# Performance work log

Measured on AMD Instinct MI355X. Metric: run time of the kernel, lower is better.

## Reference

```python
import jax, jax.numpy as jnp
import numpy as np

T = 3          # hparams['T'] message-passing iterations
E = 100000     # num edges (rows of link_state)
M = 200000     # num message pairs
D = 128        # hidden dim of link_state / GRU units
H = 256        # Message MLP hidden width
G = 64         # num graphs


def setup_inputs() -> dict:
    key = jax.random.key(0)
    ks = jax.random.split(key, 16)
    s = 0.05
    inp = {
        'link_state': jax.random.normal(ks[0], (E, D), jnp.float32),
        'states_first': jax.random.randint(ks[1], (M,), 0, E),
        'states_second': jax.random.randint(ks[2], (M,), 0, E),
        'states_graph_ids': jnp.sort(jax.random.randint(ks[3], (E,), 0, G)),
        'sates_num_edges': E,
        # Message MLP: Dense(H, relu) -> Dense(D, relu)
        'mW1': jax.random.normal(ks[4], (2 * D, H), jnp.float32) * s,
        'mb1': jnp.zeros((H,), jnp.float32),
        'mW2': jax.random.normal(ks[5], (H, D), jnp.float32) * s,
        'mb2': jnp.zeros((D,), jnp.float32),
        # GRUCell (keras, reset_after=True): kernel [D,3D], recurrent [D,3D], bias [2,3D]
        'gru_kernel': jax.random.normal(ks[6], (D, 3 * D), jnp.float32) * s,
        'gru_recurrent': jax.random.normal(ks[7], (D, 3 * D), jnp.float32) * s,
        'gru_bias': jnp.zeros((2, 3 * D), jnp.float32),
        # Readout MLP: Dense(H, relu) -> Dense(H, relu) -> Dense(1)
        'rW1': jax.random.normal(ks[8], (D, H), jnp.float32) * s,
        'rb1': jnp.zeros((H,), jnp.float32),
        'rW2': jax.random.normal(ks[9], (H, H), jnp.float32) * s,
        'rb2': jnp.zeros((H,), jnp.float32),
        'rW3': jax.random.normal(ks[10], (H, 1), jnp.float32) * s,
        'rb3': jnp.zeros((1,), jnp.float32),
    }
    return inp


def _gru_step(x, h, kernel, recurrent, bias):
    # keras GRUCell with reset_after=True; gate order: z, r, h
    mx = x @ kernel + bias[0]          # [N, 3D]
    mh = h @ recurrent + bias[1]       # [N, 3D]
    xz, xr, xh = jnp.split(mx, 3, axis=-1)
    hz, hr, hh = jnp.split(mh, 3, axis=-1)
    z = jax.nn.sigmoid(xz + hz)
    r = jax.nn.sigmoid(xr + hr)
    hcand = jnp.tanh(xh + r * hh)
    return z * h + (1.0 - z) * hcand


def reference(link_state, states_first, states_second, states_graph_ids,
              sates_num_edges, mW1, mb1, mW2, mb2,
              gru_kernel, gru_recurrent, gru_bias,
              rW1, rb1, rW2, rb2, rW3, rb3):
    for _ in range(T):
        main_e = link_state[states_first]        # [M, D] gather
        neigh_e = link_state[states_second]      # [M, D] gather
        concat = jnp.concatenate([main_e, neigh_e], axis=1)  # [M, 2D]
        msg = jax.nn.relu(concat @ mW1 + mb1)
        msg = jax.nn.relu(msg @ mW2 + mb2)       # [M, D]
        edges_inputs = jax.ops.segment_sum(msg, states_second,
                                           num_segments=sates_num_edges)  # [E, D]
        link_state = _gru_step(edges_inputs, link_state,
                               gru_kernel, gru_recurrent, gru_bias)
    graph_state = jax.ops.segment_sum(link_state, states_graph_ids,
                                      num_segments=G)  # [G, D]
    r = jax.nn.relu(graph_state @ rW1 + rb1)
    r = jax.nn.relu(r @ rW2 + rb2)
    return r @ rW3 + rb3  # [G, 1]
```

## Files before the change

### kernel.cpp

```cpp
#include <hip/hip_runtime.h>

#define NUM_E 100000
#define NUM_M 200000
#define DIM   128
#define HID   256
#define NG    64
#define TITER 3
#define NB_SCAN 98
#define GS_ER 128
#define TM    64

typedef __attribute__((ext_vector_type(8))) short bf16x8;
typedef __attribute__((ext_vector_type(4))) float f32x4;

__device__ __forceinline__ unsigned short f2bf(float f) {
  unsigned u = __float_as_uint(f);
  u += 0x7FFF + ((u >> 16) & 1);
  return (unsigned short)(u >> 16);
}
__device__ __forceinline__ float bf2f(unsigned short h) {
  return __uint_as_float(((unsigned)h) << 16);
}
__device__ __forceinline__ float sigmoidf_(float v) {
  return 1.f / (1.f + __expf(-v));
}
__device__ __forceinline__ float tanhf_(float u) {
  u = fminf(fmaxf(u, -15.f), 15.f);
  float ex = __expf(-2.f * u);
  return (1.f - ex) / (1.f + ex);
}
__device__ __forceinline__ float relu_(float v) { return fmaxf(v, 0.f); }

__device__ __forceinline__ void acc8(float* xs, bf16x8 v) {
  #pragma unroll
  for (int j = 0; j < 8; ++j) xs[j] += bf2f((unsigned short)v[j]);
}

__device__ __forceinline__ int swzm(int row, int col) {
  return row * 256 + (col ^ ((row & 7) << 3));
}
__device__ __forceinline__ int swzg(int row, int col) {
  return row * 128 + (col ^ ((row & 7) << 3));
}

#define MFMA(a, b, c) __builtin_amdgcn_mfma_f32_16x16x32_bf16((a), (b), (c), 0, 0, 0)

__global__ void hist_kernel(const int* __restrict__ second, int* __restrict__ counts,
                            float4* __restrict__ gs4) {
  int m = blockIdx.x * blockDim.x + threadIdx.x;
  if (m < NG * DIM / 4) gs4[m] = make_float4(0.f, 0.f, 0.f, 0.f);
  if (m < NUM_M) atomicAdd(&counts[second[m]], 1);
}

__global__ __launch_bounds__(256) void scan1_kernel(const int* __restrict__ counts,
                                                    int* __restrict__ partials) {
  __shared__ int sh[256];
  int b = blockIdx.x, t = threadIdx.x;
  int i0 = b * 1024 + t * 4;
  int c0 = (i0 + 0 < NUM_E) ? counts[i0 + 0] : 0;
  int c1 = (i0 + 1 < NUM_E) ? counts[i0 + 1] : 0;
  int c2 = (i0 + 2 < NUM_E) ? counts[i0 + 2] : 0;
  int c3 = (i0 + 3 < NUM_E) ? counts[i0 + 3] : 0;
  int tsum = c0 + c1 + c2 + c3;
  sh[t] = tsum;
  __syncthreads();
  for (int off = 1; off < 256; off <<= 1) {
    int v = (t >= off) ? sh[t - off] : 0;
    __syncthreads();
    sh[t] += v;
    __syncthreads();
  }
  if (t == 255) partials[b] = sh[255];
}

__global__ void scan2_kernel(const int* __restrict__ partials, int* __restrict__ base,
                             int* __restrict__ rowptr) {
  if (threadIdx.x == 0) {
    int run = 0;
    for (int b = 0; b < NB_SCAN; ++b) { base[b] = run; run += partials[b]; }
    rowptr[NUM_E] = NUM_M;
  }
}

__global__ __launch_bounds__(256) void scan3_kernel(const int* __restrict__ counts,
                                                    const int* __restrict__ base,
                                                    int* __restrict__ rowptr) {
  __shared__ int sh[256];
  int b = blockIdx.x, t = threadIdx.x;
  int i0 = b * 1024 + t * 4;
  int c0 = (i0 + 0 < NUM_E) ? counts[i0 + 0] : 0;
  int c1 = (i0 + 1 < NUM_E) ? counts[i0 + 1] : 0;
  int c2 = (i0 + 2 < NUM_E) ? counts[i0 + 2] : 0;
  int c3 = (i0 + 3 < NUM_E) ? counts[i0 + 3] : 0;
  int tsum = c0 + c1 + c2 + c3;
  sh[t] = tsum;
  __syncthreads();
  for (int off = 1; off < 256; off <<= 1) {
    int v = (t >= off) ? sh[t - off] : 0;
    __syncthreads();
    sh[t] += v;
    __syncthreads();
  }
  int p = base[b] + (sh[t] - tsum);
  if (i0 + 0 < NUM_E) rowptr[i0 + 0] = p;
  if (i0 + 1 < NUM_E) rowptr[i0 + 1] = p + c0;
  if (i0 + 2 < NUM_E) rowptr[i0 + 2] = p + c0 + c1;
  if (i0 + 3 < NUM_E) rowptr[i0 + 3] = p + c0 + c1 + c2;
}

__global__ void scatter_kernel(const int* __restrict__ second,
                               const int* __restrict__ rowptr,
                               int* __restrict__ cursor, int* __restrict__ order) {
  int m = blockIdx.x * blockDim.x + threadIdx.x;
  if (m < NUM_M) {
    int e = second[m];
    int pos = atomicAdd(&cursor[e], 1);
    int idx = rowptr[e] + pos;
    if (idx < rowptr[e + 1]) order[idx] = m;
  }
}

__device__ __forceinline__ void pack_range(
    const float* __restrict__ srcA, const float* __restrict__ srcB, int KrowsA,
    int N, int src_ld, int col_off, unsigned short* __restrict__ dst, int idx) {
  int l = idx & 63;
  int t = idx >> 6;
  int NF = N / 16;
  int nf = t % NF;
  int ks = t / NF;
  int n = nf * 16 + (l & 15) + col_off;
  int k0 = ks * 32 + (l >> 4) * 8;
  unsigned short o[8];
  #pragma unroll
  for (int j = 0; j < 8; ++j) {
    int k = k0 + j;
    const float* src = (k < KrowsA) ? (srcA + (size_t)k * src_ld)
                                    : (srcB + (size_t)(k - KrowsA) * src_ld);
    o[j] = f2bf(src[n]);
  }
  ushort4* d = (ushort4*)(dst + (size_t)idx * 8);
  d[0] = make_ushort4(o[0], o[1], o[2], o[3]);
  d[1] = make_ushort4(o[4], o[5], o[6], o[7]);
}

__global__ __launch_bounds__(256) void prep_kernel(
    const float4* __restrict__ ls4, ushort4* __restrict__ lsb4, int n4,
    const float* __restrict__ mW1, const float* __restrict__ mW2,
    const float* __restrict__ gk,  const float* __restrict__ gr,
    unsigned short* __restrict__ W1p,  unsigned short* __restrict__ W2p,
    unsigned short* __restrict__ Wzrp, unsigned short* __restrict__ Wkhp,
    unsigned short* __restrict__ Wrhp) {
  int i = blockIdx.x * 256 + threadIdx.x;
  if (i < n4) {
    float4 v = ls4[i];
    ushort4 o;
    o.x = f2bf(v.x); o.y = f2bf(v.y); o.z = f2bf(v.z); o.w = f2bf(v.w);
    lsb4[i] = o;
  }
  if      (i < 8192)  pack_range(mW1, mW1, 256, 256, 256, 0,   W1p,  i);
  else if (i < 12288) pack_range(mW2, mW2, 256, 128, 128, 0,   W2p,  i - 8192);
  else if (i < 20480) pack_range(gk,  gr,  128, 256, 384, 0,   Wzrp, i - 12288);
  else if (i < 22528) pack_range(gk,  gk,  128, 128, 384, 256, Wkhp, i - 20480);
  else if (i < 24576) pack_range(gr,  gr,  128, 128, 384, 256, Wrhp, i - 22528);
}

__global__ __launch_bounds__(512, 2) void msg_kernel(
    const unsigned short* __restrict__ lsb,
    const int* __restrict__ first, const int* __restrict__ second,
    const int* __restrict__ order,
    const unsigned short* __restrict__ W1p,
    const float* __restrict__ b1,
    const unsigned short* __restrict__ W2p,
    const float* __restrict__ b2,
    unsigned short* __restrict__ msgout)
{
  __shared__ unsigned short actL[2][TM * 256];
  __shared__ unsigned short h1s[2][TM * 256];

  const int tid  = threadIdx.x;
  const int wave = tid >> 6;
  const int lane = tid & 63;
  const int c    = lane & 15;
  const int quad = lane >> 4;

  const int sr  = tid >> 5;
  const int shf = (tid >> 4) & 1;
  const int si  = tid & 15;

  const bf16x8* W1f = (const bf16x8*)W1p;
  const bf16x8* W2f = (const bf16x8*)W2p;
  bf16x8 w1r[16];
  #pragma unroll
  for (int ks = 0; ks < 8; ++ks)
    #pragma unroll
    for (int i = 0; i < 2; ++i)
      w1r[ks * 2 + i] = W1f[(ks * 16 + wave * 2 + i) * 64 + lane];
  bf16x8 w2r[8];
  #pragma unroll
  for (int ks = 0; ks < 8; ++ks)
    w2r[ks] = W2f[(ks * 8 + wave) * 64 + lane];

  float4 b1v[2];
  #pragma unroll
  for (int i = 0; i < 2; ++i)
    b1v[i] = *(const float4*)(b1 + (wave * 2 + i) * 16 + quad * 4);
  float4 b2v = *(const float4*)(b2 + wave * 16 + quad * 4);

  const int nTiles = NUM_M / TM;
  const int stride = gridDim.x;
  int tile = blockIdx.x;
  if (tile >= nTiles) return;
  int parity = 0;

  {
    #pragma unroll
    for (int k = 0; k < 4; ++k) {
      int m = order[tile * TM + sr + k * 16];
      int e = shf ? second[m] : first[m];
      bf16x8 v = *(const bf16x8*)(lsb + (size_t)e * DIM + si * 8);
      *(bf16x8*)&actL[0][swzm(sr + k * 16, shf * 128 + si * 8)] = v;
    }
  }
  int en[4] = {0, 0, 0, 0};
  {
    int t1 = tile + stride;
    if (t1 < nTiles) {
      #pragma unroll
      for (int k = 0; k < 4; ++k) {
        int m = order[t1 * TM + sr + k * 16];
        en[k] = shf ? second[m] : first[m];
      }
    }
  }
  __syncthreads();

  while (true) {
    const int m0 = tile * TM;
    const int next  = tile + stride;
    const int next2 = next + stride;
    const bool have_next  = (next < nTiles);
    const bool have_next2 = (next2 < nTiles);

    bf16x8 sv[4];
    if (have_next) {
      #pragma unroll
      for (int k = 0; k < 4; ++k)
        sv[k] = *(const bf16x8*)(lsb + (size_t)en[k] * DIM + si * 8);
    }
    int o[4] = {0, 0, 0, 0};
    if (have_next2) {
      #pragma unroll
      for (int k = 0; k < 4; ++k)
        o[k] = order[next2 * TM + sr + k * 16];
    }

    const unsigned short* ab = &actL[parity][0];
    f32x4 acc[4][2];
    #pragma unroll
    for (int s = 0; s < 4; ++s) { acc[s][0] = (f32x4)(0.f); acc[s][1] = (f32x4)(0.f); }
    #pragma unroll
    for (int ks = 0; ks < 8; ++ks) {
      #pragma unroll
      for (int s = 0; s < 4; ++s) {
        bf16x8 b = *(const bf16x8*)&ab[swzm(s * 16 + c, ks * 32 + quad * 8)];
        acc[s][0] = MFMA(w1r[ks * 2 + 0], b, acc[s][0]);
        acc[s][1] = MFMA(w1r[ks * 2 + 1], b, acc[s][1]);
      }
    }

    if (have_next2) {
      #pragma unroll
      for (int k = 0; k < 4; ++k)
        en[k] = shf ? second[o[k]] : first[o[k]];
    }

    if (have_next) {
      unsigned short* aw = &actL[parity ^ 1][0];
      #pragma unroll
      for (int k = 0; k < 4; ++k)
        *(bf16x8*)&aw[swzm(sr + k * 16, shf * 128 + si * 8)] = sv[k];
    }

    unsigned short* hb = &h1s[parity][0];
    #pragma unroll
    for (int i = 0; i < 2; ++i) {
      int n0 = (wave * 2 + i) * 16 + quad * 4;
      #pragma unroll
      for (int s = 0; s < 4; ++s) {
        ushort4 pk;
        pk.x = f2bf(relu_(acc[s][i][0] + b1v[i].x));
        pk.y = f2bf(relu_(acc[s][i][1] + b1v[i].y));
        pk.z = f2bf(relu_(acc[s][i][2] + b1v[i].z));
        pk.w = f2bf(relu_(acc[s][i][3] + b1v[i].w));
        *(ushort4*)&hb[swzm(s * 16 + c, n0)] = pk;
      }
    }
    __syncthreads();

    f32x4 a2[4];
    #pragma unroll
    for (int s = 0; s < 4; ++s) a2[s] = (f32x4)(0.f);
    #pragma unroll
    for (int ks2 = 0; ks2 < 8; ++ks2) {
      #pragma unroll
      for (int s = 0; s < 4; ++s) {
        bf16x8 b = *(const bf16x8*)&hb[swzm(s * 16 + c, ks2 * 32 + quad * 8)];
        a2[s] = MFMA(w2r[ks2], b, a2[s]);
      }
    }

    {
      int n0 = wave * 16 + quad * 4;
      #pragma unroll
      for (int s = 0; s < 4; ++s) {
        ushort4 pk;
        pk.x = f2bf(relu_(a2[s][0] + b2v.x));
        pk.y = f2bf(relu_(a2[s][1] + b2v.y));
        pk.z = f2bf(relu_(a2[s][2] + b2v.z));
        pk.w = f2bf(relu_(a2[s][3] + b2v.w));
        *(ushort4*)(msgout + (size_t)(m0 + s * 16 + c) * DIM + n0) = pk;
      }
    }

    if (!have_next) break;
    tile = next;
    parity ^= 1;
  }
}

__device__ __forceinline__ ushort4 gru_gate(
    f32x4 az, f32x4 ar, f32x4 axh, f32x4 ahh, ushort4 hraw,
    float4 bz0, float4 br0, float4 bh0, float4 bz1, float4 br1, float4 bh1) {
  float ho[4] = { bf2f(hraw.x), bf2f(hraw.y), bf2f(hraw.z), bf2f(hraw.w) };
  const float* paz  = (const float*)&az;  const float* par  = (const float*)&ar;
  const float* paxh = (const float*)&axh; const float* pahh = (const float*)&ahh;
  const float* pz0 = (const float*)&bz0; const float* pr0 = (const float*)&br0;
  const float* ph0 = (const float*)&bh0; const float* pz1 = (const float*)&bz1;
  const float* pr1 = (const float*)&br1; const float* ph1 = (const float*)&bh1;
  unsigned short o[4];
  #pragma unroll
  for (int j = 0; j < 4; ++j) {
    float z  = sigmoidf_(paz[j] + pz0[j] + pz1[j]);
    float r  = sigmoidf_(par[j] + pr0[j] + pr1[j]);
    float hc = tanhf_(paxh[j] + ph0[j] + r * (pahh[j] + ph1[j]));
    o[j] = f2bf(z * ho[j] + (1.f - z) * hc);
  }
  return make_ushort4(o[0], o[1], o[2], o[3]);
}

__global__ __launch_bounds__(512, 2) void gru_kernel(
    const unsigned short* __restrict__ msgb,
    const int* __restrict__ rowptr,
    unsigned short* __restrict__ lsb,
    const unsigned short* __restrict__ Wzrp,
    const unsigned short* __restrict__ Wkhp,
    const unsigned short* __restrict__ Wrhp,
    const float* __restrict__ gb)
{
  __shared__ unsigned short xfL[2][32 * 128];
  __shared__ unsigned short hfL[2][32 * 128];

  const int tid  = threadIdx.x;
  const int wave = tid >> 6;
  const int lane = tid & 63;
  const int c    = lane & 15;
  const int quad = lane >> 4;

  const bf16x8* Wzrf = (const bf16x8*)Wzrp;
  const bf16x8* Wkhf = (const bf16x8*)Wkhp;
  const bf16x8* Wrhf = (const bf16x8*)Wrhp;
  bf16x8 wz[8], wr[8];
  #pragma unroll
  for (int ks = 0; ks < 8; ++ks) {
    wz[ks] = Wzrf[(ks * 16 + wave) * 64 + lane];
    wr[ks] = Wzrf[(ks * 16 + 8 + wave) * 64 + lane];
  }
  bf16x8 wxh[4], whh[4];
  #pragma unroll
  for (int ks = 0; ks < 4; ++ks) {
    wxh[ks] = Wkhf[(ks * 8 + wave) * 64 + lane];
    whh[ks] = Wrhf[(ks * 8 + wave) * 64 + lane];
  }

  const float4* gbv = (const float4*)gb;
  const int q4 = wave * 4 + quad;
  const float4 b0z = gbv[q4],      b0r = gbv[32 + q4],  b0h = gbv[64 + q4];
  const float4 b1z = gbv[96 + q4], b1r = gbv[128 + q4], b1h = gbv[160 + q4];

  const int el = wave * 4 + (lane >> 4);
  const int li = lane & 15;

  const int nTiles = NUM_E / 32;
  const int stride = gridDim.x;
  int tile = blockIdx.x;
  if (tile >= nTiles) return;
  int par = 0;

  {
    const int e  = tile * 32 + el;
    const int rs = rowptr[e], re = rowptr[e + 1];
    float xs[8];
    #pragma unroll
    for (int j = 0; j < 8; ++j) xs[j] = 0.f;
    bf16x8 hrow = *(const bf16x8*)(lsb + (size_t)e * DIM + li * 8);
    for (int p0 = rs; p0 < re; p0 += 8) {
      const int pm = re - 1;
      bf16x8 tv[8];
      #pragma unroll
      for (int k = 0; k < 8; ++k)
        tv[k] = *(const bf16x8*)(msgb + (size_t)min(p0 + k, pm) * DIM + li * 8);
      #pragma unroll
      for (int k = 0; k < 8; ++k)
        if (p0 + k < re) acc8(xs, tv[k]);
    }
    bf16x8 xv;
    #pragma unroll
    for (int j = 0; j < 8; ++j) xv[j] = (short)f2bf(xs[j]);
    *(bf16x8*)&xfL[0][swzg(el, li * 8)] = xv;
    *(bf16x8*)&hfL[0][swzg(el, li * 8)] = hrow;
  }
  int rs1 = 0, re1 = 0;
  if (tile + stride < nTiles) {
    const int e1 = (tile + stride) * 32 + el;
    rs1 = rowptr[e1]; re1 = rowptr[e1 + 1];
  }
  __syncthreads();

  while (true) {
    const int nextT = tile + stride;
    const bool have_next  = (nextT < nTiles);
    const bool have_next2 = (nextT + stride < nTiles);

    bf16x8 r0, r1, r2, r3, r4, r5, r6, r7, hrow;
    if (have_next) {
      const int e1 = nextT * 32 + el;
      const int pc = min(max(re1 - 1, rs1), NUM_M - 1);
      r0 = *(const bf16x8*)(msgb + (size_t)min(rs1 + 0, pc) * DIM + li * 8);
      r1 = *(const bf16x8*)(msgb + (size_t)min(rs1 + 1, pc) * DIM + li * 8);
      r2 = *(const bf16x8*)(msgb + (size_t)min(rs1 + 2, pc) * DIM + li * 8);
      r3 = *(const bf16x8*)(msgb + (size_t)min(rs1 + 3, pc) * DIM + li * 8);
      r4 = *(const bf16x8*)(msgb + (size_t)min(rs1 + 4, pc) * DIM + li * 8);
      r5 = *(const bf16x8*)(msgb + (size_t)min(rs1 + 5, pc) * DIM + li * 8);
      r6 = *(const bf16x8*)(msgb + (size_t)min(rs1 + 6, pc) * DIM + li * 8);
      r7 = *(const bf16x8*)(msgb + (size_t)min(rs1 + 7, pc) * DIM + li * 8);
      hrow = *(const bf16x8*)(lsb + (size_t)e1 * DIM + li * 8);
    }
    int rs2 = 0, re2 = 0;
    if (have_next2) {
      const int e2 = (nextT + stride) * 32 + el;
      rs2 = rowptr[e2]; re2 = rowptr[e2 + 1];
    }

    const unsigned short* xb = &xfL[par][0];
    const unsigned short* hb = &hfL[par][0];
    f32x4 zA = (f32x4)(0.f), zB = (f32x4)(0.f);
    f32x4 rA = (f32x4)(0.f), rB = (f32x4)(0.f);
    f32x4 xhA = (f32x4)(0.f), xhB = (f32x4)(0.f);
    f32x4 hhA = (f32x4)(0.f), hhB = (f32x4)(0.f);
    #pragma unroll
    for (int ks = 0; ks < 4; ++ks) {
      bf16x8 xA = *(const bf16x8*)&xb[swzg(c,      ks * 32 + quad * 8)];
      bf16x8 xB = *(const bf16x8*)&xb[swzg(16 + c, ks * 32 + quad * 8)];
      bf16x8 hA = *(const bf16x8*)&hb[swzg(c,      ks * 32 + quad * 8)];
      bf16x8 hB = *(const bf16x8*)&hb[swzg(16 + c, ks * 32 + quad * 8)];
      zA  = MFMA(wz[ks],     xA, zA);   zB  = MFMA(wz[ks],     xB, zB);
      rA  = MFMA(wr[ks],     xA, rA);   rB  = MFMA(wr[ks],     xB, rB);
      zA  = MFMA(wz[4 + ks], hA, zA);   zB  = MFMA(wz[4 + ks], hB, zB);
      rA  = MFMA(wr[4 + ks], hA, rA);   rB  = MFMA(wr[4 + ks], hB, rB);
      xhA = MFMA(wxh[ks],    xA, xhA);  xhB = MFMA(wxh[ks],    xB, xhB);
      hhA = MFMA(whh[ks],    hA, hhA);  hhB = MFMA(whh[ks],    hB, hhB);
    }
    {
      const int n0 = wave * 16 + quad * 4;
      ushort4 hrawA = *(const ushort4*)&hb[swzg(c,      n0)];
      ushort4 hrawB = *(const ushort4*)&hb[swzg(16 + c, n0)];
      ushort4 pkA = gru_gate(zA, rA, xhA, hhA, hrawA, b0z, b0r, b0h, b1z, b1r, b1h);
      ushort4 pkB = gru_gate(zB, rB, xhB, hhB, hrawB, b0z, b0r, b0h, b1z, b1r, b1h);
      *(ushort4*)(lsb + (size_t)(tile * 32 + c) * DIM + n0)      = pkA;
      *(ushort4*)(lsb + (size_t)(tile * 32 + 16 + c) * DIM + n0) = pkB;
    }

    if (have_next) {
      float xs[8];
      #pragma unroll
      for (int j = 0; j < 8; ++j) xs[j] = 0.f;
      if (rs1 + 0 < re1) acc8(xs, r0);
      if (rs1 + 1 < re1) acc8(xs, r1);
      if (rs1 + 2 < re1) acc8(xs, r2);
      if (rs1 + 3 < re1) acc8(xs, r3);
      if (rs1 + 4 < re1) acc8(xs, r4);
      if (rs1 + 5 < re1) acc8(xs, r5);
      if (rs1 + 6 < re1) acc8(xs, r6);
      if (rs1 + 7 < re1) acc8(xs, r7);
      for (int p0 = rs1 + 8; p0 < re1; p0 += 8) {
        const int pm = re1 - 1;
        bf16x8 tv[8];
        #pragma unroll
        for (int k = 0; k < 8; ++k)
          tv[k] = *(const bf16x8*)(msgb + (size_t)min(p0 + k, pm) * DIM + li * 8);
        #pragma unroll
        for (int k = 0; k < 8; ++k)
          if (p0 + k < re1) acc8(xs, tv[k]);
      }
      bf16x8 xv;
      #pragma unroll
      for (int j = 0; j < 8; ++j) xv[j] = (short)f2bf(xs[j]);
      *(bf16x8*)&xfL[par ^ 1][swzg(el, li * 8)] = xv;
      *(bf16x8*)&hfL[par ^ 1][swzg(el, li * 8)] = hrow;
    }
    __syncthreads();
    if (!have_next) break;
    tile = nextT;
    par ^= 1;
    rs1 = rs2;
    re1 = re2;
  }
}

__global__ __launch_bounds__(256) void graph_sum_kernel(
    const unsigned short* __restrict__ lsb, const int* __restrict__ gids,
    float* __restrict__ gs) {
  const int t = threadIdx.x;
  const int d = t & 127;
  const int half = t >> 7;
  const int e0 = blockIdx.x * GS_ER;
  const int e1 = min(e0 + GS_ER, NUM_E);
  float acc = 0.f;
  int cur = -1;
  for (int e = e0 + half; e < e1; e += 2) {
    int g = gids[e];
    if (g != cur) {
      if (cur >= 0) atomicAdd(&gs[cur * DIM + d], acc);
      acc = 0.f;
      cur = g;
    }
    acc += bf2f(lsb[(size_t)e * DIM + d]);
  }
  if (cur >= 0) atomicAdd(&gs[cur * DIM + d], acc);
}

__global__ __launch_bounds__(256) void readout_kernel(
    const float* __restrict__ gs,
    const float* __restrict__ rW1, const float* __restrict__ rb1,
    const float* __restrict__ rW2, const float* __restrict__ rb2,
    const float* __restrict__ rW3, const float* __restrict__ rb3,
    float* __restrict__ out) {
  __shared__ float shg[DIM];
  __shared__ float sh1[HID];
  __shared__ float red[HID];
  int g = blockIdx.x, c = threadIdx.x;
  if (c < DIM) shg[c] = gs[g * DIM + c];
  __syncthreads();
  float s = rb1[c];
  for (int k = 0; k < DIM; ++k) s += shg[k] * rW1[k * HID + c];
  sh1[c] = relu_(s);
  __syncthreads();
  s = rb2[c];
  for (int k = 0; k < HID; ++k) s += sh1[k] * rW2[k * HID + c];
  red[c] = relu_(s) * rW3[c];
  __syncthreads();
  for (int off = 128; off > 0; off >>= 1) {
    if (c < off) red[c] += red[c + off];
    __syncthreads();
  }
  if (c == 0) out[g] = red[0] + rb3[0];
}

extern "C" void kernel_launch(void* const* d_in, const int* in_sizes, int n_in,
                              void* d_out, int out_size, void* d_ws, size_t ws_size,
                              hipStream_t stream) {
  float* ls          = (float*)d_in[0];
  const int* first   = (const int*)d_in[1];
  const int* second  = (const int*)d_in[2];
  const int* gids    = (const int*)d_in[3];
  const float* mW1   = (const float*)d_in[5];
  const float* mb1   = (const float*)d_in[6];
  const float* mW2   = (const float*)d_in[7];
  const float* mb2   = (const float*)d_in[8];
  const float* gk    = (const float*)d_in[9];
  const float* gr    = (const float*)d_in[10];
  const float* gb    = (const float*)d_in[11];
  const float* rW1   = (const float*)d_in[12];
  const float* rb1   = (const float*)d_in[13];
  const float* rW2   = (const float*)d_in[14];
  const float* rb2   = (const float*)d_in[15];
  const float* rW3   = (const float*)d_in[16];
  const float* rb3   = (const float*)d_in[17];
  float* out = (float*)d_out;

  char* w = (char*)d_ws;
  unsigned short* msgb = (unsigned short*)w;    w += (size_t)NUM_M * DIM * 2;
  unsigned short* lsb  = (unsigned short*)w;    w += (size_t)NUM_E * DIM * 2;
  float* gs    = (float*)w;                     w += NG * DIM * 4;
  int* counts  = (int*)w;                       w += NUM_E * 4;
  int* cursor  = (int*)w;                       w += NUM_E * 4;
  int* rowptr  = (int*)w;                       w += (NUM_E + 4) * 4;
  int* order   = (int*)w;                       w += NUM_M * 4;
  int* partials= (int*)w;                       w += NB_SCAN * 4;
  int* basep   = (int*)w;                       w += NB_SCAN * 4;
  unsigned short* W1p  = (unsigned short*)w;    w += 256 * 256 * 2;
  unsigned short* W2p  = (unsigned short*)w;    w += 256 * 128 * 2;
  unsigned short* Wzrp = (unsigned short*)w;    w += 256 * 256 * 2;
  unsigned short* Wkhp = (unsigned short*)w;    w += 128 * 128 * 2;
  unsigned short* Wrhp = (unsigned short*)w;    w += 128 * 128 * 2;

  const int n4 = NUM_E * DIM / 4;
  prep_kernel<<<(n4 + 255) / 256, 256, 0, stream>>>(
      (const float4*)ls, (ushort4*)lsb, n4, mW1, mW2, gk, gr,
      W1p, W2p, Wzrp, Wkhp, Wrhp);

  hipMemsetAsync(counts, 0, 2 * (size_t)NUM_E * 4, stream);
  hist_kernel<<<(NUM_M + 255) / 256, 256, 0, stream>>>(second, counts, (float4*)gs);
  scan1_kernel<<<NB_SCAN, 256, 0, stream>>>(counts, partials);
  scan2_kernel<<<1, 64, 0, stream>>>(partials, basep, rowptr);
  scan3_kernel<<<NB_SCAN, 256, 0, stream>>>(counts, basep, rowptr);
  scatter_kernel<<<(NUM_M + 255) / 256, 256, 0, stream>>>(second, rowptr, cursor, order);

  for (int t = 0; t < TITER; ++t) {
    msg_kernel<<<256, 512, 0, stream>>>(lsb, first, second, order, W1p, mb1, W2p, mb2, msgb);
    gru_kernel<<<256, 512, 0, stream>>>(msgb, rowptr, lsb, Wzrp, Wkhp, Wrhp, gb);
  }
  graph_sum_kernel<<<(NUM_E + GS_ER - 1) / GS_ER, 256, 0, stream>>>(lsb, gids, gs);
  readout_kernel<<<NG, HID, 0, stream>>>(gs, rW1, rb1, rW2, rb2, rW3, rb3, out);
}
```

Baseline: 495.4 us.

## Double GRU tile to 64 edges and fold histogram into prep kernel

The GRU kernel now handles 64 edges per tile in two 32-row sub-groups. Each sub-group's segment-sum prefetch for the next tile is interleaved with the current sub-group's MFMA work, and the kernel syncs once per 64 rows instead of once per 32. The edge-count histogram and graph-sum zeroing move into prep_kernel, removing one launch. The larger LDS buffers and extra live registers may lower occupancy, and a tail clamp is added for the partial last tile.

```diff
diff --git a/kernel.cpp b/kernel.cpp
--- a/kernel.cpp
+++ b/kernel.cpp
@@ -9,6 +9,7 @@
 #define NB_SCAN 98
 #define GS_ER 128
 #define TM    64
+#define TMG   64
 
 typedef __attribute__((ext_vector_type(8))) short bf16x8;
 typedef __attribute__((ext_vector_type(4))) float f32x4;
@@ -44,13 +45,6 @@
 }
 
 #define MFMA(a, b, c) __builtin_amdgcn_mfma_f32_16x16x32_bf16((a), (b), (c), 0, 0, 0)
-
-__global__ void hist_kernel(const int* __restrict__ second, int* __restrict__ counts,
-                            float4* __restrict__ gs4) {
-  int m = blockIdx.x * blockDim.x + threadIdx.x;
-  if (m < NG * DIM / 4) gs4[m] = make_float4(0.f, 0.f, 0.f, 0.f);
-  if (m < NUM_M) atomicAdd(&counts[second[m]], 1);
-}
 
 __global__ __launch_bounds__(256) void scan1_kernel(const int* __restrict__ counts,
                                                     int* __restrict__ partials) {
@@ -145,6 +139,8 @@
 
 __global__ __launch_bounds__(256) void prep_kernel(
     const float4* __restrict__ ls4, ushort4* __restrict__ lsb4, int n4,
+    const int* __restrict__ second, int* __restrict__ counts,
+    float4* __restrict__ gs4,
     const float* __restrict__ mW1, const float* __restrict__ mW2,
     const float* __restrict__ gk,  const float* __restrict__ gr,
     unsigned short* __restrict__ W1p,  unsigned short* __restrict__ W2p,
@@ -157,6 +153,8 @@
     o.x = f2bf(v.x); o.y = f2bf(v.y); o.z = f2bf(v.z); o.w = f2bf(v.w);
     lsb4[i] = o;
   }
+  if (i < NUM_M) atomicAdd(&counts[second[i]], 1);
+  if (i < NG * DIM / 4) gs4[i] = make_float4(0.f, 0.f, 0.f, 0.f);
   if      (i < 8192)  pack_range(mW1, mW1, 256, 256, 256, 0,   W1p,  i);
   else if (i < 12288) pack_range(mW2, mW2, 256, 128, 128, 0,   W2p,  i - 8192);
   else if (i < 20480) pack_range(gk,  gr,  128, 256, 384, 0,   Wzrp, i - 12288);
@@ -357,8 +355,8 @@
     const unsigned short* __restrict__ Wrhp,
     const float* __restrict__ gb)
 {
-  __shared__ unsigned short xfL[2][32 * 128];
-  __shared__ unsigned short hfL[2][32 * 128];
+  __shared__ unsigned short xfL[2][TMG * 128];
+  __shared__ unsigned short hfL[2][TMG * 128];
 
   const int tid  = threadIdx.x;
   const int wave = tid >> 6;
@@ -390,19 +388,21 @@
   const int el = wave * 4 + (lane >> 4);
   const int li = lane & 15;
 
-  const int nTiles = NUM_E / 32;
+  const int nTiles = (NUM_E + TMG - 1) / TMG;
   const int stride = gridDim.x;
   int tile = blockIdx.x;
   if (tile >= nTiles) return;
   int par = 0;
 
-  {
-    const int e  = tile * 32 + el;
-    const int rs = rowptr[e], re = rowptr[e + 1];
+  #pragma unroll
+  for (int g = 0; g < 2; ++g) {
+    const int e  = tile * TMG + g * 32 + el;
+    const int ec = min(e, NUM_E - 1);
+    const int rs = rowptr[ec], re = rowptr[ec + 1];
     float xs[8];
     #pragma unroll
     for (int j = 0; j < 8; ++j) xs[j] = 0.f;
-    bf16x8 hrow = *(const bf16x8*)(lsb + (size_t)e * DIM + li * 8);
+    bf16x8 hrow = *(const bf16x8*)(lsb + (size_t)ec * DIM + li * 8);
     for (int p0 = rs; p0 < re; p0 += 8) {
       const int pm = re - 1;
       bf16x8 tv[8];
@@ -416,13 +416,16 @@
     bf16x8 xv;
     #pragma unroll
     for (int j = 0; j < 8; ++j) xv[j] = (short)f2bf(xs[j]);
-    *(bf16x8*)&xfL[0][swzg(el, li * 8)] = xv;
-    *(bf16x8*)&hfL[0][swzg(el, li * 8)] = hrow;
-  }
-  int rs1 = 0, re1 = 0;
+    *(bf16x8*)&xfL[0][swzg(g * 32 + el, li * 8)] = xv;
+    *(bf16x8*)&hfL[0][swzg(g * 32 + el, li * 8)] = hrow;
+  }
+  int rs1[2] = {0, 0}, re1[2] = {0, 0};
   if (tile + stride < nTiles) {
-    const int e1 = (tile + stride) * 32 + el;
-    rs1 = rowptr[e1]; re1 = rowptr[e1 + 1];
+    #pragma unroll
+    for (int g = 0; g < 2; ++g) {
+      const int e1 = min((tile + stride) * TMG + g * 32 + el, NUM_E - 1);
+      rs1[g] = rowptr[e1]; re1[g] = rowptr[e1 + 1];
+    }
   }
   __syncthreads();
 
@@ -431,89 +434,99 @@
     const bool have_next  = (nextT < nTiles);
     const bool have_next2 = (nextT + stride < nTiles);
 
-    bf16x8 r0, r1, r2, r3, r4, r5, r6, r7, hrow;
-    if (have_next) {
-      const int e1 = nextT * 32 + el;
-      const int pc = min(max(re1 - 1, rs1), NUM_M - 1);
-      r0 = *(const bf16x8*)(msgb + (size_t)min(rs1 + 0, pc) * DIM + li * 8);
-      r1 = *(const bf16x8*)(msgb + (size_t)min(rs1 + 1, pc) * DIM + li * 8);
-      r2 = *(const bf16x8*)(msgb + (size_t)min(rs1 + 2, pc) * DIM + li * 8);
-      r3 = *(const bf16x8*)(msgb + (size_t)min(rs1 + 3, pc) * DIM + li * 8);
-      r4 = *(const bf16x8*)(msgb + (size_t)min(rs1 + 4, pc) * DIM + li * 8);
-      r5 = *(const bf16x8*)(msgb + (size_t)min(rs1 + 5, pc) * DIM + li * 8);
-      r6 = *(const bf16x8*)(msgb + (size_t)min(rs1 + 6, pc) * DIM + li * 8);
-      r7 = *(const bf16x8*)(msgb + (size_t)min(rs1 + 7, pc) * DIM + li * 8);
-      hrow = *(const bf16x8*)(lsb + (size_t)e1 * DIM + li * 8);
-    }
-    int rs2 = 0, re2 = 0;
+    int rs2[2] = {0, 0}, re2[2] = {0, 0};
     if (have_next2) {
-      const int e2 = (nextT + stride) * 32 + el;
-      rs2 = rowptr[e2]; re2 = rowptr[e2 + 1];
+      #pragma unroll
+      for (int g = 0; g < 2; ++g) {
+        const int e2 = min((nextT + stride) * TMG + g * 32 + el, NUM_E - 1);
+        rs2[g] = rowptr[e2]; re2[g] = rowptr[e2 + 1];
+      }
     }
 
     const unsigned short* xb = &xfL[par][0];
     const unsigned short* hb = &hfL[par][0];
-    f32x4 zA = (f32x4)(0.f), zB = (f32x4)(0.f);
-    f32x4 rA = (f32x4)(0.f), rB = (f32x4)(0.f);
-    f32x4 xhA = (f32x4)(0.f), xhB = (f32x4)(0.f);
-    f32x4 hhA = (f32x4)(0.f), hhB = (f32x4)(0.f);
-    #pragma unroll
-    for (int ks = 0; ks < 4; ++ks) {
-      bf16x8 xA = *(const bf16x8*)&xb[swzg(c,      ks * 32 + quad * 8)];
-      bf16x8 xB = *(const bf16x8*)&xb[swzg(16 + c, ks * 32 + quad * 8)];
-      bf16x8 hA = *(const bf16x8*)&hb[swzg(c,      ks * 32 + quad * 8)];
-      bf16x8 hB = *(const bf16x8*)&hb[swzg(16 + c, ks * 32 + quad * 8)];
-      zA  = MFMA(wz[ks],     xA, zA);   zB  = MFMA(wz[ks],     xB, zB);
-      rA  = MFMA(wr[ks],     xA, rA);   rB  = MFMA(wr[ks],     xB, rB);
-      zA  = MFMA(wz[4 + ks], hA, zA);   zB  = MFMA(wz[4 + ks], hB, zB);
-      rA  = MFMA(wr[4 + ks], hA, rA);   rB  = MFMA(wr[4 + ks], hB, rB);
-      xhA = MFMA(wxh[ks],    xA, xhA);  xhB = MFMA(wxh[ks],    xB, xhB);
-      hhA = MFMA(whh[ks],    hA, hhA);  hhB = MFMA(whh[ks],    hB, hhB);
-    }
-    {
-      const int n0 = wave * 16 + quad * 4;
-      ushort4 hrawA = *(const ushort4*)&hb[swzg(c,      n0)];
-      ushort4 hrawB = *(const ushort4*)&hb[swzg(16 + c, n0)];
-      ushort4 pkA = gru_gate(zA, rA, xhA, hhA, hrawA, b0z, b0r, b0h, b1z, b1r, b1h);
-      ushort4 pkB = gru_gate(zB, rB, xhB, hhB, hrawB, b0z, b0r, b0h, b1z, b1r, b1h);
-      *(ushort4*)(lsb + (size_t)(tile * 32 + c) * DIM + n0)      = pkA;
-      *(ushort4*)(lsb + (size_t)(tile * 32 + 16 + c) * DIM + n0) = pkB;
-    }
-
-    if (have_next) {
-      float xs[8];
-      #pragma unroll
-      for (int j = 0; j < 8; ++j) xs[j] = 0.f;
-      if (rs1 + 0 < re1) acc8(xs, r0);
-      if (rs1 + 1 < re1) acc8(xs, r1);
-      if (rs1 + 2 < re1) acc8(xs, r2);
-      if (rs1 + 3 < re1) acc8(xs, r3);
-      if (rs1 + 4 < re1) acc8(xs, r4);
-      if (rs1 + 5 < re1) acc8(xs, r5);
-      if (rs1 + 6 < re1) acc8(xs, r6);
-      if (rs1 + 7 < re1) acc8(xs, r7);
-      for (int p0 = rs1 + 8; p0 < re1; p0 += 8) {
-        const int pm = re1 - 1;
-        bf16x8 tv[8];
+
+    #pragma unroll
+    for (int g = 0; g < 2; ++g) {
+      bf16x8 r0, r1, r2, r3, r4, r5, r6, r7, hrow;
+      if (have_next) {
+        const int e1 = min(nextT * TMG + g * 32 + el, NUM_E - 1);
+        const int pc = min(max(re1[g] - 1, rs1[g]), NUM_M - 1);
+        r0 = *(const bf16x8*)(msgb + (size_t)min(rs1[g] + 0, pc) * DIM + li * 8);
+        r1 = *(const bf16x8*)(msgb + (size_t)min(rs1[g] + 1, pc) * DIM + li * 8);
+        r2 = *(const bf16x8*)(msgb + (size_t)min(rs1[g] + 2, pc) * DIM + li * 8);
+        r3 = *(const bf16x8*)(msgb + (size_t)min(rs1[g] + 3, pc) * DIM + li * 8);
+        r4 = *(const bf16x8*)(msgb + (size_t)min(rs1[g] + 4, pc) * DIM + li * 8);
+        r5 = *(const bf16x8*)(msgb + (size_t)min(rs1[g] + 5, pc) * DIM + li * 8);
+        r6 = *(const bf16x8*)(msgb + (size_t)min(rs1[g] + 6, pc) * DIM + li * 8);
+        r7 = *(const bf16x8*)(msgb + (size_t)min(rs1[g] + 7, pc) * DIM + li * 8);
+        hrow = *(const bf16x8*)(lsb + (size_t)e1 * DIM + li * 8);
+      }
+
+      f32x4 zA = (f32x4)(0.f), zB = (f32x4)(0.f);
+      f32x4 rA = (f32x4)(0.f), rB = (f32x4)(0.f);
+      f32x4 xhA = (f32x4)(0.f), xhB = (f32x4)(0.f);
+      f32x4 hhA = (f32x4)(0.f), hhB = (f32x4)(0.f);
+      #pragma unroll
+      for (int ks = 0; ks < 4; ++ks) {
+        bf16x8 xA = *(const bf16x8*)&xb[swzg(g * 32 + c,      ks * 32 + quad * 8)];
+        bf16x8 xB = *(const bf16x8*)&xb[swzg(g * 32 + 16 + c, ks * 32 + quad * 8)];
+        bf16x8 hA = *(const bf16x8*)&hb[swzg(g * 32 + c,      ks * 32 + quad * 8)];
+        bf16x8 hB = *(const bf16x8*)&hb[swzg(g * 32 + 16 + c, ks * 32 + quad * 8)];
+        zA  = MFMA(wz[ks],     xA, zA);   zB  = MFMA(wz[ks],     xB, zB);
+        rA  = MFMA(wr[ks],     xA, rA);   rB  = MFMA(wr[ks],     xB, rB);
+        zA  = MFMA(wz[4 + ks], hA, zA);   zB  = MFMA(wz[4 + ks], hB, zB);
+        rA  = MFMA(wr[4 + ks], hA, rA);   rB  = MFMA(wr[4 + ks], hB, rB);
+        xhA = MFMA(wxh[ks],    xA, xhA);  xhB = MFMA(wxh[ks],    xB, xhB);
+        hhA = MFMA(whh[ks],    hA, hhA);  hhB = MFMA(whh[ks],    hB, hhB);
+      }
+      {
+        const int n0 = wave * 16 + quad * 4;
+        const int eA = tile * TMG + g * 32 + c;
+        const int eB = tile * TMG + g * 32 + 16 + c;
+        ushort4 hrawA = *(const ushort4*)&hb[swzg(g * 32 + c,      n0)];
+        ushort4 hrawB = *(const ushort4*)&hb[swzg(g * 32 + 16 + c, n0)];
+        ushort4 pkA = gru_gate(zA, rA, xhA, hhA, hrawA, b0z, b0r, b0h, b1z, b1r, b1h);
+        ushort4 pkB = gru_gate(zB, rB, xhB, hhB, hrawB, b0z, b0r, b0h, b1z, b1r, b1h);
+        if (eA < NUM_E) *(ushort4*)(lsb + (size_t)eA * DIM + n0) = pkA;
+        if (eB < NUM_E) *(ushort4*)(lsb + (size_t)eB * DIM + n0) = pkB;
+      }
+
+      if (have_next) {
+        float xs[8];
         #pragma unroll
-        for (int k = 0; k < 8; ++k)
-          tv[k] = *(const bf16x8*)(msgb + (size_t)min(p0 + k, pm) * DIM + li * 8);
+        for (int j = 0; j < 8; ++j) xs[j] = 0.f;
+        if (rs1[g] + 0 < re1[g]) acc8(xs, r0);
+        if (rs1[g] + 1 < re1[g]) acc8(xs, r1);
+        if (rs1[g] + 2 < re1[g]) acc8(xs, r2);
+        if (rs1[g] + 3 < re1[g]) acc8(xs, r3);
+        if (rs1[g] + 4 < re1[g]) acc8(xs, r4);
+        if (rs1[g] + 5 < re1[g]) acc8(xs, r5);
+        if (rs1[g] + 6 < re1[g]) acc8(xs, r6);
+        if (rs1[g] + 7 < re1[g]) acc8(xs, r7);
+        for (int p0 = rs1[g] + 8; p0 < re1[g]; p0 += 8) {
+          const int pm = re1[g] - 1;
+          bf16x8 tv[8];
+          #pragma unroll
+          for (int k = 0; k < 8; ++k)
+            tv[k] = *(const bf16x8*)(msgb + (size_t)min(p0 + k, pm) * DIM + li * 8);
+          #pragma unroll
+          for (int k = 0; k < 8; ++k)
+            if (p0 + k < re1[g]) acc8(xs, tv[k]);
+        }
+        bf16x8 xv;
         #pragma unroll
-        for (int k = 0; k < 8; ++k)
-          if (p0 + k < re1) acc8(xs, tv[k]);
-      }
-      bf16x8 xv;
-      #pragma unroll
-      for (int j = 0; j < 8; ++j) xv[j] = (short)f2bf(xs[j]);
-      *(bf16x8*)&xfL[par ^ 1][swzg(el, li * 8)] = xv;
-      *(bf16x8*)&hfL[par ^ 1][swzg(el, li * 8)] = hrow;
+        for (int j = 0; j < 8; ++j) xv[j] = (short)f2bf(xs[j]);
+        *(bf16x8*)&xfL[par ^ 1][swzg(g * 32 + el, li * 8)] = xv;
+        *(bf16x8*)&hfL[par ^ 1][swzg(g * 32 + el, li * 8)] = hrow;
+      }
     }
     __syncthreads();
     if (!have_next) break;
     tile = nextT;
     par ^= 1;
-    rs1 = rs2;
-    re1 = re2;
+    rs1[0] = rs2[0]; re1[0] = re2[0];
+    rs1[1] = rs2[1]; re1[1] = re2[1];
   }
 }
 
@@ -604,13 +617,12 @@
   unsigned short* Wkhp = (unsigned short*)w;    w += 128 * 128 * 2;
   unsigned short* Wrhp = (unsigned short*)w;    w += 128 * 128 * 2;
 
+  hipMemsetAsync(counts, 0, 2 * (size_t)NUM_E * 4, stream);
   const int n4 = NUM_E * DIM / 4;
   prep_kernel<<<(n4 + 255) / 256, 256, 0, stream>>>(
-      (const float4*)ls, (ushort4*)lsb, n4, mW1, mW2, gk, gr,
-      W1p, W2p, Wzrp, Wkhp, Wrhp);
-
-  hipMemsetAsync(counts, 0, 2 * (size_t)NUM_E * 4, stream);
-  hist_kernel<<<(NUM_M + 255) / 256, 256, 0, stream>>>(second, counts, (float4*)gs);
+      (const float4*)ls, (ushort4*)lsb, n4, second, counts, (float4*)gs,
+      mW1, mW2, gk, gr, W1p, W2p, Wzrp, Wkhp, Wrhp);
+
   scan1_kernel<<<NB_SCAN, 256, 0, stream>>>(counts, partials);
   scan2_kernel<<<1, 64, 0, stream>>>(partials, basep, rowptr);
   scan3_kernel<<<NB_SCAN, 256, 0, stream>>>(counts, basep, rowptr);
```

Result: slower. 512.4 us (+3.4%).
